# Kernel tuning notes

Measured on AMD Instinct MI355X. Metric: run time of the kernel, lower is better.

## Reference

```python
import jax, jax.numpy as jnp
import numpy as np
import math

NUM_HEADS = 16
HEAD_SIZE = 64
QKT_MEAN = 0.0
QKT_STD = 0.05
APPLY_NOISE = True
NOISE_KEY = jax.random.key(42)


def quantize_activation_8bit(x):
    max_abs = jnp.maximum(jnp.max(jnp.abs(x)), 1e-08)
    scale = max_abs / 127.0
    return jnp.clip(jnp.round(x / scale), -127, 127) * scale


def quantize_weight_4bit(w):
    max_abs = jnp.maximum(jnp.max(jnp.abs(w)), 1e-08)
    scale = max_abs / 7.0
    return jnp.clip(jnp.round(w / scale), -7, 7) * scale


def setup_inputs() -> dict:
    key = jax.random.key(0)
    k1, k2, k3, k4 = jax.random.split(key, 4)
    B, S, D = 4, 1024, 1024
    hidden_states = jax.random.normal(k1, (B, S, D), dtype=jnp.float32)
    attention_mask = jnp.zeros((B, 1, 1, S), dtype=jnp.float32)
    # nn.Linear weights are [out_features, in_features]
    w_scale = 1.0 / math.sqrt(D)
    Wq = jax.random.normal(k2, (D, D), dtype=jnp.float32) * w_scale
    Wk = jax.random.normal(k3, (D, D), dtype=jnp.float32) * w_scale
    Wv = jax.random.normal(k4, (D, D), dtype=jnp.float32) * w_scale
    return {"hidden_states": hidden_states, "attention_mask": attention_mask,
            "Wq": Wq, "Wk": Wk, "Wv": Wv}


def _split_heads(x):
    B, S, _ = x.shape
    return x.reshape(B, S, NUM_HEADS, HEAD_SIZE).transpose(0, 2, 1, 3)  # [B,H,S,Dh]


def reference(hidden_states, attention_mask, Wq, Wk, Wv):
    h_q = quantize_activation_8bit(hidden_states)
    h_k = quantize_activation_8bit(hidden_states)
    Q = _split_heads(jnp.einsum('bsd,od->bso', h_q, quantize_weight_4bit(Wq)))
    K = _split_heads(jnp.einsum('bsd,od->bso', h_k, quantize_weight_4bit(Wk)))
    V = _split_heads(jnp.einsum('bsd,od->bso', hidden_states, quantize_weight_4bit(Wv)))
    qkt = jnp.einsum('bhqd,bhkd->bhqk', Q, K) / math.sqrt(HEAD_SIZE)
    if APPLY_NOISE and QKT_STD > 0:
        noise = jax.random.normal(NOISE_KEY, qkt.shape, dtype=qkt.dtype) * QKT_STD + QKT_MEAN
        qkt = qkt + noise
    qkt = qkt + attention_mask  # [B,1,1,S] broadcasts over [B,H,S,S]
    attn_weights = jax.nn.softmax(qkt, axis=-1)  # dropout is identity in eval
    ctx = jnp.einsum('bhqk,bhkd->bhqd', attn_weights, V)
    B, H, S, Dh = ctx.shape
    ctx = ctx.transpose(0, 2, 1, 3).reshape(B, S, H * Dh)
    return ctx
```

## Files before the change

### kernel.cpp

```cpp
#include <hip/hip_runtime.h>
#include <hip/hip_bf16.h>

typedef unsigned short u16;
typedef unsigned int u32;
typedef __bf16 bf16x8 __attribute__((ext_vector_type(8)));
typedef float f32x4 __attribute__((ext_vector_type(4)));

#define MFMA16(a, b, c) __builtin_amdgcn_mfma_f32_16x16x32_bf16((a), (b), (c), 0, 0, 0)

static __device__ __forceinline__ float bfbits2f(u32 b) {
    union { u32 u; float f; } c; c.u = b << 16; return c.f;
}
static __device__ __forceinline__ u32 f2bfbits(float f) {
    union { float f; u32 u; } c; c.f = f;
    return (c.u + 0x7FFFu + ((c.u >> 16) & 1u)) >> 16;
}
static __device__ __forceinline__ u32 f2bfbits_exact(float f) {
    union { float f; u32 u; } c; c.f = f;
    return c.u >> 16;
}
static __device__ __forceinline__ u32 pack_bf16x2(float lo, float hi) {
    float2 v; v.x = lo; v.y = hi;
    union { __hip_bfloat162 h; u32 u; } c;
    c.h = __float22bfloat162_rn(v);
    return c.u;
}

static __device__ __forceinline__ void noise_pu8(const u32* __restrict__ idx,
                                                 float* __restrict__ pu) {
    const u32 K1 = 42u, K2 = 0x1BD11BF0u;
    u32 x0[8], x1[8];
#pragma unroll
    for (int d = 0; d < 8; d++) { x0[d] = 0u; x1[d] = idx[d] + K1; }
#define TFR(R)                                            \
    _Pragma("unroll") for (int d = 0; d < 8; d++) {       \
        x0[d] += x1[d];                                   \
        x1[d] = __builtin_rotateleft32(x1[d], R) ^ x0[d]; \
    }
#define INJ(A, B)                                         \
    _Pragma("unroll") for (int d = 0; d < 8; d++) {       \
        x0[d] += (A); x1[d] += (B);                       \
    }
    TFR(13) TFR(15) TFR(26) TFR(6)  INJ(K1, K2 + 1u)
    TFR(17) TFR(29) TFR(16) TFR(24) INJ(K2, 2u)
    TFR(13) TFR(15) TFR(26) TFR(6)  INJ(0u, K1 + 3u)
    TFR(17) TFR(29) TFR(16) TFR(24) INJ(K1, K2 + 4u)
    TFR(13) TFR(15) TFR(26) TFR(6)  INJ(K2, 5u)
#undef TFR
#undef INJ
#pragma unroll
    for (int d = 0; d < 8; d++) {
        u32 bits = x0[d] ^ x1[d];
        float f = __uint_as_float((bits >> 9) | 0x3F800000u) - 1.0f;
        float u = fmaf(f, 2.0f, -0.99999994f);
        u = fmaxf(-0.99999994f, u);
        float t = fmaf(-u, u, 1.0f);
        float lg = __logf(t);
        float p;
        if (lg > -5.0f) {
            float z = fmaf(lg, -1.0f, -2.5f);
            p = 2.81022636e-08f;
            p = fmaf(p, z, 3.43273939e-07f);
            p = fmaf(p, z, -3.5233877e-06f);
            p = fmaf(p, z, -4.39150654e-06f);
            p = fmaf(p, z, 0.00021858087f);
            p = fmaf(p, z, -0.00125372503f);
            p = fmaf(p, z, -0.00417768164f);
            p = fmaf(p, z, 0.246640727f);
            p = fmaf(p, z, 1.50140941f);
        } else {
            float z = sqrtf(-lg) - 3.0f;
            p = -0.000200214257f;
            p = fmaf(p, z, 0.000100950558f);
            p = fmaf(p, z, 0.00134934322f);
            p = fmaf(p, z, -0.00367342844f);
            p = fmaf(p, z, 0.00573950773f);
            p = fmaf(p, z, -0.0076224613f);
            p = fmaf(p, z, 0.00943887047f);
            p = fmaf(p, z, 1.00167406f);
            p = fmaf(p, z, 2.83297682f);
        }
        pu[d] = p * u;
    }
}

__global__ __launch_bounds__(256) void absmax_k(const float* __restrict__ h,
                                                const float* __restrict__ wq,
                                                const float* __restrict__ wk,
                                                const float* __restrict__ wv,
                                                u32* __restrict__ slots) {
    int t = blockIdx.y;
    const float* src = (t == 0) ? h : (t == 1) ? wq : (t == 2) ? wk : wv;
    int n4 = ((t == 0) ? 4096 * 1024 : 1024 * 1024) / 4;
    u32 mx = 0;
    int tid = threadIdx.x;
    for (int i = blockIdx.x * blockDim.x + tid; i < n4; i += gridDim.x * blockDim.x) {
        uint4 v = ((const uint4*)src)[i];
        mx = max(mx, v.x & 0x7FFFFFFFu);
        mx = max(mx, v.y & 0x7FFFFFFFu);
        mx = max(mx, v.z & 0x7FFFFFFFu);
        mx = max(mx, v.w & 0x7FFFFFFFu);
    }
    __shared__ u32 red[256];
    red[tid] = mx;
    __syncthreads();
    for (int s = 128; s > 0; s >>= 1) {
        if (tid < s) red[tid] = max(red[tid], red[tid + s]);
        __syncthreads();
    }
    if (tid == 0) atomicMax(&slots[t], red[0]);
}

__global__ __launch_bounds__(256) void prequant_all(const float* __restrict__ hidden,
                                                    const float* __restrict__ wq,
                                                    const float* __restrict__ wk,
                                                    const float* __restrict__ wv,
                                                    u16* __restrict__ hq,
                                                    u16* __restrict__ hbf,
                                                    u16* __restrict__ wqi,
                                                    u16* __restrict__ wki,
                                                    u16* __restrict__ wvi,
                                                    const u32* __restrict__ slots) {
    int y = blockIdx.y;
    const float* src = (y == 0) ? hidden : (y == 1) ? wq : (y == 2) ? wk : wv;
    u16* dqi = (y == 0) ? hq : (y == 1) ? wqi : (y == 2) ? wki : wvi;
    u16* draw = (y == 0) ? hbf : nullptr;
    float qmax = (y == 0) ? 127.0f : 7.0f;
    int n8 = ((y == 0) ? 4096 * 1024 : 1024 * 1024) / 8;

    float amax = fmaxf(__uint_as_float(slots[y]), 1e-8f);
    float scale = amax / qmax;
    for (int i = blockIdx.x * blockDim.x + threadIdx.x; i < n8; i += gridDim.x * blockDim.x) {
        float4 a = ((const float4*)src)[2 * i];
        float4 b = ((const float4*)src)[2 * i + 1];
        float x[8] = {a.x, a.y, a.z, a.w, b.x, b.y, b.z, b.w};
        u16 qi[8], rw[8];
#pragma unroll
        for (int j = 0; j < 8; j++) {
            float q = fminf(fmaxf(rintf(x[j] / scale), -qmax), qmax);
            qi[j] = (u16)f2bfbits_exact(q);
            rw[j] = (u16)f2bfbits(x[j]);
        }
        *(uint4*)(dqi + 8 * (size_t)i) = *(const uint4*)qi;
        if (draw) *(uint4*)(draw + 8 * (size_t)i) = *(const uint4*)rw;
    }
}

__global__ __launch_bounds__(256) void qkv_gemm_all(const u16* __restrict__ hq,
                                                    const u16* __restrict__ hbf,
                                                    const u16* __restrict__ wqi,
                                                    const u16* __restrict__ wki,
                                                    const u16* __restrict__ wvi,
                                                    const u32* __restrict__ slots,
                                                    u16* __restrict__ Qb,
                                                    u16* __restrict__ Kb,
                                                    u16* __restrict__ Vtb) {
    __shared__ __align__(16) u16 As[64 * 40];
    __shared__ __align__(16) u16 Bs[64 * 40];
    int z = blockIdx.z;
    const u16* A  = (z < 2) ? hq : hbf;
    const u16* Bw = (z == 0) ? wqi : (z == 1) ? wki : wvi;
    u16* outp     = (z == 0) ? Qb : (z == 1) ? Kb : Vtb;
    int transOut = (z == 2);
    float s_a = fmaxf(__uint_as_float(slots[0]), 1e-8f) / 127.0f;
    float s_w = fmaxf(__uint_as_float(slots[z + 1]), 1e-8f) / 7.0f;
    float oscale = (z < 2) ? (s_a * s_w) : s_w;

    int tid = threadIdx.x;
    int srow = tid >> 2, scol = (tid & 3) * 8;
    int mbase = blockIdx.x * 64, nbase = blockIdx.y * 64;
    int lane = tid & 63, wv = tid >> 6;
    int quad = lane >> 4, l16 = lane & 15;

    f32x4 acc[4];
#pragma unroll
    for (int i = 0; i < 4; i++) acc[i] = (f32x4){0.f, 0.f, 0.f, 0.f};

    const u16* aptr = A + (size_t)(mbase + srow) * 1024 + scol;
    const u16* bptr = Bw + (size_t)(nbase + srow) * 1024 + scol;

    for (int k0 = 0; k0 < 1024; k0 += 32) {
        uint4 av = *(const uint4*)(aptr + k0);
        uint4 bv = *(const uint4*)(bptr + k0);
        __syncthreads();
        *(uint4*)(As + srow * 40 + scol) = av;
        *(uint4*)(Bs + srow * 40 + scol) = bv;
        __syncthreads();
        bf16x8 af = *(const bf16x8*)(As + (wv * 16 + l16) * 40 + quad * 8);
#pragma unroll
        for (int nt = 0; nt < 4; nt++) {
            bf16x8 bfr = *(const bf16x8*)(Bs + (nt * 16 + l16) * 40 + quad * 8);
            acc[nt] = MFMA16(af, bfr, acc[nt]);
        }
    }

#pragma unroll
    for (int nt = 0; nt < 4; nt++) {
#pragma unroll
        for (int r = 0; r < 4; r++) {
            float val = acc[nt][r] * oscale;
            int m = mbase + wv * 16 + quad * 4 + r;
            int o = nbase + nt * 16 + l16;
            int b = m >> 10, s = m & 1023;
            int hh = o >> 6, dh = o & 63;
            size_t off = transOut ? (((size_t)(b * 16 + hh) * 64 + dh) * 1024 + s)
                                  : (((size_t)(b * 16 + hh) * 1024 + s) * 64 + dh);
            outp[off] = (u16)f2bfbits(val);
        }
    }
}

__global__ __launch_bounds__(256, 2) void attn_kernel(const u16* __restrict__ Q,
                                                      const u16* __restrict__ K,
                                                      const u16* __restrict__ Vt,
                                                      const float* __restrict__ mask,
                                                      float* __restrict__ outp) {
    __shared__ __align__(16) u16 Plds[2][4][16][40];
    int qt = blockIdx.x, h = blockIdx.y, b = blockIdx.z;
    int bh = b * 16 + h;
    int tid = threadIdx.x, wv = tid >> 6, lane = tid & 63;
    int quad = lane >> 4, l16 = lane & 15;
    int q0 = qt * 64 + wv * 16;

    const u16* Qb = Q + (size_t)bh * 1024 * 64;
    const u16* Kb = K + (size_t)bh * 1024 * 64;
    const u16* Vb = Vt + (size_t)bh * 64 * 1024;

    bf16x8 aq0 = *(const bf16x8*)(Qb + (q0 + l16) * 64 + quad * 8);
    bf16x8 aq1 = *(const bf16x8*)(Qb + (q0 + l16) * 64 + 32 + quad * 8);

    f32x4 oacc[4];
#pragma unroll
    for (int i = 0; i < 4; i++) oacc[i] = (f32x4){0.f, 0.f, 0.f, 0.f};
    float lsum[4] = {0.f, 0.f, 0.f, 0.f};

    u16* Pw0 = &Plds[0][wv][0][0];
    u16* Pw1 = &Plds[1][wv][0][0];
    u32 idxbase = ((u32)bh * 1024u + (u32)(q0 + quad * 4)) * 1024u;
    const float* maskb = mask + b * 1024;

    for (int ks = 0; ks < 1024; ks += 32) {
        f32x4 s0 = (f32x4){0.f, 0.f, 0.f, 0.f};
        f32x4 s1 = (f32x4){0.f, 0.f, 0.f, 0.f};
        const u16* Kt = Kb + (size_t)ks * 64;
        bf16x8 bk0 = *(const bf16x8*)(Kt + l16 * 64 + quad * 8);
        bf16x8 bk1 = *(const bf16x8*)(Kt + l16 * 64 + 32 + quad * 8);
        bf16x8 bk2 = *(const bf16x8*)(Kt + (16 + l16) * 64 + quad * 8);
        bf16x8 bk3 = *(const bf16x8*)(Kt + (16 + l16) * 64 + 32 + quad * 8);
        s0 = MFMA16(aq0, bk0, s0);
        s0 = MFMA16(aq1, bk1, s0);
        s1 = MFMA16(aq0, bk2, s1);
        s1 = MFMA16(aq1, bk3, s1);

        int kg0 = ks + l16;
        float mk0 = maskb[kg0];
        float mk1 = maskb[kg0 + 16];

        u32 idxs[8];
        float pu[8];
#pragma unroll
        for (int r = 0; r < 4; r++) {
            u32 idx = idxbase + (u32)r * 1024u + (u32)kg0;
            idxs[2 * r] = idx;
            idxs[2 * r + 1] = idx + 16u;
        }
        noise_pu8(idxs, pu);

        u16* myP = ((ks >> 5) & 1) ? Pw1 : Pw0;
#pragma unroll
        for (int r = 0; r < 4; r++) {
            float sv0 = fmaf(pu[2 * r], 0.07071067811865475f, fmaf(s0[r], 0.125f, mk0));
            float sv1 = fmaf(pu[2 * r + 1], 0.07071067811865475f, fmaf(s1[r], 0.125f, mk1));
            u32 pk = pack_bf16x2(__expf(sv0), __expf(sv1));
            myP[(quad * 4 + r) * 40 + l16] = (u16)pk;
            myP[(quad * 4 + r) * 40 + 16 + l16] = (u16)(pk >> 16);
            lsum[r] += bfbits2f(pk & 0xFFFFu) + bfbits2f(pk >> 16);
        }

        asm volatile("" ::: "memory");
        bf16x8 pf = *(const bf16x8*)(myP + l16 * 40 + quad * 8);
        asm volatile("" ::: "memory");
        const u16* Vk = Vb + ks;
#pragma unroll
        for (int nt = 0; nt < 4; nt++) {
            bf16x8 vf = *(const bf16x8*)(Vk + (nt * 16 + l16) * 1024 + quad * 8);
            oacc[nt] = MFMA16(pf, vf, oacc[nt]);
        }
    }

    float linv[4];
#pragma unroll
    for (int r = 0; r < 4; r++) {
        float l = lsum[r];
        l += __shfl_xor(l, 1);
        l += __shfl_xor(l, 2);
        l += __shfl_xor(l, 4);
        l += __shfl_xor(l, 8);
        linv[r] = 1.0f / l;
    }
#pragma unroll
    for (int nt = 0; nt < 4; nt++) {
#pragma unroll
        for (int r = 0; r < 4; r++) {
            int q = q0 + quad * 4 + r;
            int dh = nt * 16 + l16;
            outp[((size_t)(b * 1024 + q)) * 1024 + h * 64 + dh] = oacc[nt][r] * linv[r];
        }
    }
}

extern "C" void kernel_launch(void* const* d_in, const int* in_sizes, int n_in,
                              void* d_out, int out_size, void* d_ws, size_t ws_size,
                              hipStream_t stream) {
    (void)in_sizes; (void)n_in; (void)out_size; (void)ws_size;
    const float* hidden = (const float*)d_in[0];
    const float* maskp  = (const float*)d_in[1];
    const float* Wq     = (const float*)d_in[2];
    const float* Wk     = (const float*)d_in[3];
    const float* Wv     = (const float*)d_in[4];
    float* outp = (float*)d_out;

    char* ws = (char*)d_ws;
    u32* slots = (u32*)ws;
    u16* hq  = (u16*)(ws + 256);
    u16* hbf = hq + 4096 * 1024;
    u16* wqi = hbf + 4096 * 1024;
    u16* wki = wqi + 1024 * 1024;
    u16* wvi = wki + 1024 * 1024;
    u16* Qb  = wvi + 1024 * 1024;
    u16* Kb  = Qb + 4096 * 1024;
    u16* Vtb = Kb + 4096 * 1024;

    hipMemsetAsync(slots, 0, 16, stream);
    absmax_k<<<dim3(128, 4), 256, 0, stream>>>(hidden, Wq, Wk, Wv, slots);
    prequant_all<<<dim3(64, 4), 256, 0, stream>>>(hidden, Wq, Wk, Wv,
                                                  hq, hbf, wqi, wki, wvi, slots);
    qkv_gemm_all<<<dim3(64, 16, 3), 256, 0, stream>>>(hq, hbf, wqi, wki, wvi, slots,
                                                      Qb, Kb, Vtb);
    attn_kernel<<<dim3(16, 16, 4), 256, 0, stream>>>(Qb, Kb, Vtb, maskp, outp);
}
```

Baseline: 395.4 us.

## Split attention key range in two and combine partial outputs in a separate kernel

The attention kernel now processes half of the key sequence per block, doubling the grid. Each half writes unnormalized partial outputs and row sums to separate buffers, reusing dead workspace regions. A new combine kernel adds the partials and divides by the summed row sums. This trades an extra output-sized write, a read-back pass and one more launch for more independent blocks, which could help scheduling and the tail of the grid.

```diff
diff --git a/kernel.cpp b/kernel.cpp
--- a/kernel.cpp
+++ b/kernel.cpp
@@ -214,13 +214,21 @@
                                                       const u16* __restrict__ K,
                                                       const u16* __restrict__ Vt,
                                                       const float* __restrict__ mask,
-                                                      float* __restrict__ outp) {
+                                                      float* __restrict__ O0,
+                                                      float* __restrict__ O1,
+                                                      float* __restrict__ l0,
+                                                      float* __restrict__ l1) {
     __shared__ __align__(16) u16 Plds[2][4][16][40];
-    int qt = blockIdx.x, h = blockIdx.y, b = blockIdx.z;
+    int qt = blockIdx.x, h = blockIdx.y;
+    int b = blockIdx.z & 3, split = blockIdx.z >> 2;
     int bh = b * 16 + h;
     int tid = threadIdx.x, wv = tid >> 6, lane = tid & 63;
     int quad = lane >> 4, l16 = lane & 15;
     int q0 = qt * 64 + wv * 16;
+    int ks0 = split * 512;
+
+    float* Obuf = split ? O1 : O0;
+    float* lbuf = split ? l1 : l0;
 
     const u16* Qb = Q + (size_t)bh * 1024 * 64;
     const u16* Kb = K + (size_t)bh * 1024 * 64;
@@ -239,7 +247,7 @@
     u32 idxbase = ((u32)bh * 1024u + (u32)(q0 + quad * 4)) * 1024u;
     const float* maskb = mask + b * 1024;
 
-    for (int ks = 0; ks < 1024; ks += 32) {
+    for (int ks = ks0; ks < ks0 + 512; ks += 32) {
         f32x4 s0 = (f32x4){0.f, 0.f, 0.f, 0.f};
         f32x4 s1 = (f32x4){0.f, 0.f, 0.f, 0.f};
         const u16* Kt = Kb + (size_t)ks * 64;
@@ -288,7 +296,7 @@
         }
     }
 
-    float linv[4];
+    float lred[4];
 #pragma unroll
     for (int r = 0; r < 4; r++) {
         float l = lsum[r];
@@ -296,7 +304,12 @@
         l += __shfl_xor(l, 2);
         l += __shfl_xor(l, 4);
         l += __shfl_xor(l, 8);
-        linv[r] = 1.0f / l;
+        lred[r] = l;
+    }
+    if (l16 == 0) {
+        int lbase = bh * 1024 + q0 + quad * 4;
+#pragma unroll
+        for (int r = 0; r < 4; r++) lbuf[lbase + r] = lred[r];
     }
 #pragma unroll
     for (int nt = 0; nt < 4; nt++) {
@@ -304,9 +317,30 @@
         for (int r = 0; r < 4; r++) {
             int q = q0 + quad * 4 + r;
             int dh = nt * 16 + l16;
-            outp[((size_t)(b * 1024 + q)) * 1024 + h * 64 + dh] = oacc[nt][r] * linv[r];
-        }
-    }
+            Obuf[((size_t)(b * 1024 + q)) * 1024 + h * 64 + dh] = oacc[nt][r];
+        }
+    }
+}
+
+__global__ __launch_bounds__(256) void combine_k(float* __restrict__ outp,
+                                                 const float* __restrict__ O1,
+                                                 const float* __restrict__ l0,
+                                                 const float* __restrict__ l1) {
+    int gid = blockIdx.x * 256 + threadIdx.x;
+    int e = gid << 2;
+    int bq = e >> 10;
+    int h = (e & 1023) >> 6;
+    int b = bq >> 10, q = bq & 1023;
+    int lidx = ((b * 16 + h) << 10) + q;
+    float linv = 1.0f / (l0[lidx] + l1[lidx]);
+    float4 a = ((const float4*)outp)[gid];
+    float4 c = ((const float4*)O1)[gid];
+    float4 o;
+    o.x = (a.x + c.x) * linv;
+    o.y = (a.y + c.y) * linv;
+    o.z = (a.z + c.z) * linv;
+    o.w = (a.w + c.w) * linv;
+    ((float4*)outp)[gid] = o;
 }
 
 extern "C" void kernel_launch(void* const* d_in, const int* in_sizes, int n_in,
@@ -331,11 +365,17 @@
     u16* Kb  = Qb + 4096 * 1024;
     u16* Vtb = Kb + 4096 * 1024;
 
+    float* O1buf = (float*)hq;
+    float* l0buf = (float*)wqi;
+    float* l1buf = l0buf + 4 * 16 * 1024;
+
     hipMemsetAsync(slots, 0, 16, stream);
     absmax_k<<<dim3(128, 4), 256, 0, stream>>>(hidden, Wq, Wk, Wv, slots);
     prequant_all<<<dim3(64, 4), 256, 0, stream>>>(hidden, Wq, Wk, Wv,
                                                   hq, hbf, wqi, wki, wvi, slots);
     qkv_gemm_all<<<dim3(64, 16, 3), 256, 0, stream>>>(hq, hbf, wqi, wki, wvi, slots,
                                                       Qb, Kb, Vtb);
-    attn_kernel<<<dim3(16, 16, 4), 256, 0, stream>>>(Qb, Kb, Vtb, maskp, outp);
-}
+    attn_kernel<<<dim3(16, 16, 8), 256, 0, stream>>>(Qb, Kb, Vtb, maskp,
+                                                     outp, O1buf, l0buf, l1buf);
+    combine_k<<<dim3(4096), 256, 0, stream>>>(outp, O1buf, l0buf, l1buf);
+}
```

New measurement: 389.2 us. About the same (-1.6%).
